# Kernel optimization log

Measured on AMD Instinct MI355X. Metric: run time of the kernel, lower is better.

## Reference

```python
import jax, jax.numpy as jnp
from jax import lax
import numpy as np

EPS = 1e-5
RADIUS = 0.2
NPOINT = 1024
NSAMPLE = 32
B, N = 8, 8192


def furthest_point_sample(xyz, npoint):
    # xyz: (B,N,3) -> idx (B,npoint), start at index 0 (pytorch3d default)
    Bn, Nn, _ = xyz.shape
    def step(carry, _):
        dists, last = carry  # (B,N), (B,)
        lastpt = jnp.take_along_axis(xyz, last[:, None, None], axis=1)  # (B,1,3)
        d = jnp.sum((xyz - lastpt) ** 2, axis=-1)  # (B,N)
        dists = jnp.minimum(dists, d)
        nxt = jnp.argmax(dists, axis=-1).astype(jnp.int32)
        return (dists, nxt), last
    init = (jnp.full((Bn, Nn), jnp.inf, xyz.dtype), jnp.zeros((Bn,), jnp.int32))
    _, idxs = lax.scan(step, init, None, length=npoint)  # (npoint,B)
    return idxs.T  # (B,npoint)


def ball_query(radius, nsample, xyz, new_xyz):
    # first `nsample` points (by original index order) within radius; pad -> 0 (clamp of -1)
    Nn = xyz.shape[1]
    d2 = jnp.sum((new_xyz[:, :, None, :] - xyz[:, None, :, :]) ** 2, axis=-1)  # (B,S,N)
    valid = d2 < radius * radius
    score = jnp.where(valid, jnp.arange(Nn, dtype=jnp.int32), jnp.int32(Nn))  # smaller = earlier valid
    neg_vals, _ = lax.top_k(-score, nsample)  # picks nsample smallest scores
    idx = -neg_vals  # (B,S,nsample)
    idx = jnp.where(idx == Nn, 0, idx)  # pytorch3d pads with -1, then clamp(min=0) -> 0
    return idx


def bn_relu(x, g, be, m, v):
    # eval-mode BatchNorm over channel (last) dim + ReLU
    return jax.nn.relu((x - m) * (g / jnp.sqrt(v + EPS)) + be)


def setup_inputs() -> dict:
    key = jax.random.key(0)
    ks = jax.random.split(key, 4)
    xyz = jax.random.uniform(ks[0], (B, N, 3), dtype=jnp.float32)
    w1 = jax.random.normal(ks[1], (64, 3), dtype=jnp.float32) * 0.1
    w2 = jax.random.normal(ks[2], (64, 64), dtype=jnp.float32) * 0.1
    w3 = jax.random.normal(ks[3], (128, 64), dtype=jnp.float32) * 0.1
    z64, o64 = jnp.zeros((64,), jnp.float32), jnp.ones((64,), jnp.float32)
    z128, o128 = jnp.zeros((128,), jnp.float32), jnp.ones((128,), jnp.float32)
    return {
        "xyz": xyz,
        "w1": w1, "b1": z64, "g1": o64, "be1": z64, "m1": z64, "v1": o64,
        "w2": w2, "b2": z64, "g2": o64, "be2": z64, "m2": z64, "v2": o64,
        "w3": w3, "b3": z128, "g3": o128, "be3": z128, "m3": z128, "v3": o128,
    }


def reference(xyz, w1, b1, g1, be1, m1, v1, w2, b2, g2, be2, m2, v2, w3, b3, g3, be3, m3, v3):
    fps_idx = furthest_point_sample(xyz, NPOINT)  # (B,npoint)
    new_xyz = jnp.take_along_axis(xyz, fps_idx[:, :, None], axis=1)  # (B,npoint,3)
    idx = ball_query(RADIUS, NSAMPLE, xyz, new_xyz)  # (B,npoint,nsample)
    grouped_xyz = jax.vmap(lambda pts, i: pts[i])(xyz, idx)  # (B,npoint,nsample,3)
    # 1x1 conv MLP (channels-last) + eval BN + ReLU
    h = bn_relu(jnp.einsum('bsnc,oc->bsno', grouped_xyz, w1) + b1, g1, be1, m1, v1)
    h = bn_relu(jnp.einsum('bsnc,oc->bsno', h, w2) + b2, g2, be2, m2, v2)
    h = bn_relu(jnp.einsum('bsnc,oc->bsno', h, w3) + b3, g3, be3, m3, v3)
    new_features = jnp.max(h, axis=2)  # (B,npoint,128) max over nsample
    new_features = jnp.transpose(new_features, (0, 2, 1))  # (B,128,npoint) to match torch layout
    return new_xyz, new_features
```

## Files before the change

### kernel.cpp

```cpp
#include <hip/hip_runtime.h>

#define B 8
#define N 8192
#define S 1024
#define NS 32
constexpr float BN_EPS = 1e-5f;

typedef float v2f __attribute__((ext_vector_type(2)));

__device__ __forceinline__ float wave_max_to_lane63(float x) {
  int v = __float_as_int(x);
#define DPP_MAX(ctrl)                                                     \
  v = __float_as_int(fmaxf(__int_as_float(v),                             \
      __int_as_float(__builtin_amdgcn_update_dpp(v, v, (ctrl), 0xf, 0xf, \
                                                 false))))
  DPP_MAX(0x111);
  DPP_MAX(0x112);
  DPP_MAX(0x114);
  DPP_MAX(0x118);
  DPP_MAX(0x142);
  DPP_MAX(0x143);
#undef DPP_MAX
  return __int_as_float(v);
}

#define FPS_T 512

__global__ void __attribute__((amdgpu_flat_work_group_size(FPS_T, FPS_T),
                               amdgpu_waves_per_eu(2, 2)))
k_fps(const float* __restrict__ xyz, float* __restrict__ new_xyz) {
#pragma clang fp contract(off)
  extern __shared__ float s_xyz[];
  const int b = blockIdx.x;
  const int t = threadIdx.x;
  const int lane = t & 63;
  const int w = t >> 6;
  const float* base = xyz + (size_t)b * N * 3;
  v2f X[8], Y[8], Z[8], D[8];
  const int p0 = t * 16;
  {
    const float4* src = (const float4*)(base + (size_t)p0 * 3);
    float4* dst = (float4*)(s_xyz + (size_t)p0 * 3);
    float buf[48];
#pragma unroll
    for (int i = 0; i < 12; ++i) {
      float4 v = src[i];
      dst[i] = v;
      buf[4 * i + 0] = v.x; buf[4 * i + 1] = v.y;
      buf[4 * i + 2] = v.z; buf[4 * i + 3] = v.w;
    }
#pragma unroll
    for (int i = 0; i < 8; ++i) {
      X[i] = (v2f){buf[6 * i + 0], buf[6 * i + 3]};
      Y[i] = (v2f){buf[6 * i + 1], buf[6 * i + 4]};
      Z[i] = (v2f){buf[6 * i + 2], buf[6 * i + 5]};
      D[i] = (v2f){3.4e38f, 3.4e38f};
    }
  }
  __shared__ unsigned long long s_red[2][8];
  float lx = base[0], ly = base[1], lz = base[2];
  if (t == 0) {
    float* o = new_xyz + (size_t)b * S * 3;
    o[0] = lx; o[1] = ly; o[2] = lz;
  }
  for (int r = 1; r < S; ++r) {
    v2f lx2 = lx, ly2 = ly, lz2 = lz;
#pragma unroll
    for (int i = 0; i < 8; ++i) {
      v2f dx = X[i] - lx2, dy = Y[i] - ly2, dz = Z[i] - lz2;
      v2f d = (dx * dx + dy * dy) + dz * dz;
      D[i].x = fminf(D[i].x, d.x);
      D[i].y = fminf(D[i].y, d.y);
    }
    float m = fmaxf(D[0].x, D[0].y);
#pragma unroll
    for (int i = 1; i < 8; ++i) m = fmaxf(m, fmaxf(D[i].x, D[i].y));
    int li = 0;
#pragma unroll
    for (int i = 7; i >= 0; --i) {
      if (D[i].y == m) li = 2 * i + 1;
      if (D[i].x == m) li = 2 * i;
    }
    float wm = wave_max_to_lane63(m);
    float wavemax = __int_as_float(
        __builtin_amdgcn_readlane(__float_as_int(wm), 63));
    unsigned long long bal = __ballot(m == wavemax);
    int firstlane = (int)__builtin_ctzll(bal);
    int widx = __builtin_amdgcn_readlane(p0 + li, firstlane);
    unsigned long long key =
        ((unsigned long long)__float_as_uint(wavemax) << 32) |
        (unsigned)(8191 - widx);
    if (lane == 0) s_red[r & 1][w] = key;
    __syncthreads();
    unsigned long long k0 = s_red[r & 1][0];
#pragma unroll
    for (int j = 1; j < 8; ++j) {
      unsigned long long kj = s_red[r & 1][j];
      if (kj > k0) k0 = kj;
    }
    const int bi = 8191 - (int)(unsigned)(k0 & 0xffffffffull);
    lx = s_xyz[bi * 3 + 0];
    ly = s_xyz[bi * 3 + 1];
    lz = s_xyz[bi * 3 + 2];
    if (t == 0) {
      float* o = new_xyz + ((size_t)b * S + r) * 3;
      o[0] = lx; o[1] = ly; o[2] = lz;
    }
  }
}

__global__ __launch_bounds__(256) void k_ball(const float* __restrict__ xyz,
                                              const float* __restrict__ new_xyz,
                                              int* __restrict__ ball_idx) {
#pragma clang fp contract(off)
  constexpr float R2 = (float)(0.2 * 0.2);
  const int t = threadIdx.x;
  const int wv = (blockIdx.x << 2) + (t >> 6);
  const int lane = t & 63;
  const int b = wv >> 10;
  const float* base = xyz + (size_t)b * N * 3;
  const float* c = new_xyz + (size_t)wv * 3;
  float cx = c[0], cy = c[1], cz = c[2];
  int* out = ball_idx + (size_t)wv * NS;
  int cnt = 0;
  for (int c0 = 0; c0 < N && cnt < NS; c0 += 64) {
    int p = c0 + lane;
    float x = base[p * 3], y = base[p * 3 + 1], z = base[p * 3 + 2];
    float dx = x - cx, dy = y - cy, dz = z - cz;
    float d = (dx * dx + dy * dy) + dz * dz;
    bool v = d < R2;
    unsigned long long mk = __ballot(v);
    int rank = cnt + __popcll(mk & ((1ull << lane) - 1ull));
    if (v && rank < NS) out[rank] = p;
    cnt += (int)__popcll(mk);
  }
  if (cnt < NS)
    for (int j = cnt + lane; j < NS; j += 64) out[j] = 0;
}

__global__ void __attribute__((amdgpu_flat_work_group_size(256, 256),
                               amdgpu_waves_per_eu(2, 2)))
k_mlp(const float* __restrict__ xyz, const int* __restrict__ ball_idx,
      const float* __restrict__ w1, const float* __restrict__ b1,
      const float* __restrict__ g1, const float* __restrict__ be1,
      const float* __restrict__ m1, const float* __restrict__ v1,
      const float* __restrict__ w2, const float* __restrict__ b2,
      const float* __restrict__ g2, const float* __restrict__ be2,
      const float* __restrict__ m2, const float* __restrict__ v2,
      const float* __restrict__ w3, const float* __restrict__ b3,
      const float* __restrict__ g3, const float* __restrict__ be3,
      const float* __restrict__ m3, const float* __restrict__ v3,
      float* __restrict__ out_feat) {
  const int t = threadIdx.x;
  const int w = t >> 6, lane = t & 63;
  const int wv = (blockIdx.x << 2) + w;
  const int b = wv >> 10, s = wv & (S - 1);
  __shared__ float sh[4][NS * 64];
  __shared__ float sc[4][NS * 4];
  float* h = sh[w];
  float* cs = sc[w];
  const int* gi = ball_idx + (size_t)wv * NS;
  const float* base = xyz + (size_t)b * N * 3;
  if (lane < NS) {
    int p = gi[lane];
    cs[lane * 4 + 0] = base[p * 3 + 0];
    cs[lane * 4 + 1] = base[p * 3 + 1];
    cs[lane * 4 + 2] = base[p * 3 + 2];
  }
  __syncthreads();
  {
    float sv = g1[lane] / sqrtf(v1[lane] + BN_EPS);
    float bb = (b1[lane] - m1[lane]) * sv + be1[lane];
    float wx = w1[lane * 3 + 0] * sv, wy = w1[lane * 3 + 1] * sv,
          wz = w1[lane * 3 + 2] * sv;
    for (int n = 0; n < NS; ++n) {
      float a = fmaf(wx, cs[n * 4 + 0],
                     fmaf(wy, cs[n * 4 + 1], fmaf(wz, cs[n * 4 + 2], bb)));
      h[n * 64 + lane] = fmaxf(a, 0.f);
    }
  }
  __syncthreads();
  {
    float sv = g2[lane] / sqrtf(v2[lane] + BN_EPS);
    float bb = (b2[lane] - m2[lane]) * sv + be2[lane];
    float W[64];
#pragma unroll
    for (int k = 0; k < 64; k += 4) {
      float4 q = *(const float4*)(w2 + lane * 64 + k);
      W[k + 0] = q.x * sv; W[k + 1] = q.y * sv;
      W[k + 2] = q.z * sv; W[k + 3] = q.w * sv;
    }
    for (int n = 0; n < NS; ++n) {
      float acc = bb;
#pragma unroll
      for (int k = 0; k < 64; k += 4) {
        float4 q = *(const float4*)(h + n * 64 + k);
        acc = fmaf(W[k + 0], q.x, acc);
        acc = fmaf(W[k + 1], q.y, acc);
        acc = fmaf(W[k + 2], q.z, acc);
        acc = fmaf(W[k + 3], q.w, acc);
      }
      h[n * 64 + lane] = fmaxf(acc, 0.f);
    }
  }
  __syncthreads();
  float mxa = 0.f, mxb = 0.f;
  {
    float sva = g3[lane] / sqrtf(v3[lane] + BN_EPS);
    float bba = (b3[lane] - m3[lane]) * sva + be3[lane];
    float svb = g3[lane + 64] / sqrtf(v3[lane + 64] + BN_EPS);
    float bbb = (b3[lane + 64] - m3[lane + 64]) * svb + be3[lane + 64];
    float Wa[64], Wb[64];
#pragma unroll
    for (int k = 0; k < 64; k += 4) {
      float4 qa = *(const float4*)(w3 + lane * 64 + k);
      Wa[k + 0] = qa.x * sva; Wa[k + 1] = qa.y * sva;
      Wa[k + 2] = qa.z * sva; Wa[k + 3] = qa.w * sva;
      float4 qb = *(const float4*)(w3 + (lane + 64) * 64 + k);
      Wb[k + 0] = qb.x * svb; Wb[k + 1] = qb.y * svb;
      Wb[k + 2] = qb.z * svb; Wb[k + 3] = qb.w * svb;
    }
    for (int n = 0; n < NS; ++n) {
      float acca = bba, accb = bbb;
#pragma unroll
      for (int k = 0; k < 64; k += 4) {
        float4 q = *(const float4*)(h + n * 64 + k);
        acca = fmaf(Wa[k + 0], q.x, acca);
        acca = fmaf(Wa[k + 1], q.y, acca);
        acca = fmaf(Wa[k + 2], q.z, acca);
        acca = fmaf(Wa[k + 3], q.w, acca);
        accb = fmaf(Wb[k + 0], q.x, accb);
        accb = fmaf(Wb[k + 1], q.y, accb);
        accb = fmaf(Wb[k + 2], q.z, accb);
        accb = fmaf(Wb[k + 3], q.w, accb);
      }
      mxa = fmaxf(mxa, acca);
      mxb = fmaxf(mxb, accb);
    }
  }
  out_feat[((size_t)b * 128 + lane) * S + s] = mxa;
  out_feat[((size_t)b * 128 + 64 + lane) * S + s] = mxb;
}

extern "C" void kernel_launch(void* const* d_in, const int* in_sizes, int n_in,
                              void* d_out, int out_size, void* d_ws,
                              size_t ws_size, hipStream_t stream) {
  const float* xyz = (const float*)d_in[0];
  const float* w1 = (const float*)d_in[1];
  const float* b1 = (const float*)d_in[2];
  const float* g1 = (const float*)d_in[3];
  const float* be1 = (const float*)d_in[4];
  const float* m1 = (const float*)d_in[5];
  const float* v1 = (const float*)d_in[6];
  const float* w2 = (const float*)d_in[7];
  const float* b2 = (const float*)d_in[8];
  const float* g2 = (const float*)d_in[9];
  const float* be2 = (const float*)d_in[10];
  const float* m2 = (const float*)d_in[11];
  const float* v2 = (const float*)d_in[12];
  const float* w3 = (const float*)d_in[13];
  const float* b3 = (const float*)d_in[14];
  const float* g3 = (const float*)d_in[15];
  const float* be3 = (const float*)d_in[16];
  const float* m3 = (const float*)d_in[17];
  const float* v3 = (const float*)d_in[18];

  float* out = (float*)d_out;
  float* new_xyz = out;
  float* out_feat = out + (size_t)B * S * 3;
  int* ball = (int*)d_ws;

  k_fps<<<B, FPS_T, N * 3 * sizeof(float), stream>>>(xyz, new_xyz);
  k_ball<<<(B * S) / 4, 256, 0, stream>>>(xyz, new_xyz, ball);
  k_mlp<<<(B * S) / 4, 256, 0, stream>>>(xyz, ball, w1, b1, g1, be1, m1, v1,
                                         w2, b2, g2, be2, m2, v2, w3, b3, g3,
                                         be3, m3, v3, out_feat);
}
```

Measured before the change: 1.113 ms.

## Shorten FPS iteration critical path with tree argmax and padded float4 LDS

```diff
diff --git a/kernel.cpp b/kernel.cpp
--- a/kernel.cpp
+++ b/kernel.cpp
@@ -30,7 +30,9 @@
                                amdgpu_waves_per_eu(2, 2)))
 k_fps(const float* __restrict__ xyz, float* __restrict__ new_xyz) {
 #pragma clang fp contract(off)
-  extern __shared__ float s_xyz[];
+  extern __shared__ float4 s_xyz4[];
+  __shared__ alignas(16) float s_ctr[S * 3];
+  __shared__ unsigned long long s_red[2][8];
   const int b = blockIdx.x;
   const int t = threadIdx.x;
   const int lane = t & 63;
@@ -40,14 +42,17 @@
   const int p0 = t * 16;
   {
     const float4* src = (const float4*)(base + (size_t)p0 * 3);
-    float4* dst = (float4*)(s_xyz + (size_t)p0 * 3);
     float buf[48];
 #pragma unroll
     for (int i = 0; i < 12; ++i) {
       float4 v = src[i];
-      dst[i] = v;
       buf[4 * i + 0] = v.x; buf[4 * i + 1] = v.y;
       buf[4 * i + 2] = v.z; buf[4 * i + 3] = v.w;
+    }
+#pragma unroll
+    for (int k = 0; k < 16; ++k) {
+      s_xyz4[p0 + k] =
+          make_float4(buf[3 * k], buf[3 * k + 1], buf[3 * k + 2], 0.f);
     }
 #pragma unroll
     for (int i = 0; i < 8; ++i) {
@@ -57,11 +62,9 @@
       D[i] = (v2f){3.4e38f, 3.4e38f};
     }
   }
-  __shared__ unsigned long long s_red[2][8];
   float lx = base[0], ly = base[1], lz = base[2];
   if (t == 0) {
-    float* o = new_xyz + (size_t)b * S * 3;
-    o[0] = lx; o[1] = ly; o[2] = lz;
+    s_ctr[0] = lx; s_ctr[1] = ly; s_ctr[2] = lz;
   }
   for (int r = 1; r < S; ++r) {
     v2f lx2 = lx, ly2 = ly, lz2 = lz;
@@ -69,18 +72,32 @@
     for (int i = 0; i < 8; ++i) {
       v2f dx = X[i] - lx2, dy = Y[i] - ly2, dz = Z[i] - lz2;
       v2f d = (dx * dx + dy * dy) + dz * dz;
-      D[i].x = fminf(D[i].x, d.x);
-      D[i].y = fminf(D[i].y, d.y);
-    }
-    float m = fmaxf(D[0].x, D[0].y);
-#pragma unroll
-    for (int i = 1; i < 8; ++i) m = fmaxf(m, fmaxf(D[i].x, D[i].y));
-    int li = 0;
-#pragma unroll
-    for (int i = 7; i >= 0; --i) {
-      if (D[i].y == m) li = 2 * i + 1;
-      if (D[i].x == m) li = 2 * i;
-    }
+      D[i] = __builtin_elementwise_min(D[i], d);
+    }
+    float n1[8], n2[4], n3[2];
+#pragma unroll
+    for (int i = 0; i < 8; ++i) n1[i] = fmaxf(D[i].x, D[i].y);
+#pragma unroll
+    for (int i = 0; i < 4; ++i) n2[i] = fmaxf(n1[2 * i], n1[2 * i + 1]);
+    n3[0] = fmaxf(n2[0], n2[1]);
+    n3[1] = fmaxf(n2[2], n2[3]);
+    float m = fmaxf(n3[0], n3[1]);
+    int c3 = (n3[0] < m) ? 1 : 0;
+    float n2s = c3 ? n2[2] : n2[0];
+    int c2 = (n2s < m) ? 1 : 0;
+    float n1a = c3 ? n1[4] : n1[0];
+    float n1b = c3 ? n1[6] : n1[2];
+    float n1s = c2 ? n1b : n1a;
+    int c1 = (n1s < m) ? 1 : 0;
+    float dx0 = c3 ? D[4].x : D[0].x;
+    float dx1 = c3 ? D[5].x : D[1].x;
+    float dx2 = c3 ? D[6].x : D[2].x;
+    float dx3 = c3 ? D[7].x : D[3].x;
+    float dxa = c2 ? dx2 : dx0;
+    float dxb = c2 ? dx3 : dx1;
+    float dxs = c1 ? dxb : dxa;
+    int c0 = (dxs < m) ? 1 : 0;
+    int li = 8 * c3 + 4 * c2 + 2 * c1 + c0;
     float wm = wave_max_to_lane63(m);
     float wavemax = __int_as_float(
         __builtin_amdgcn_readlane(__float_as_int(wm), 63));
@@ -92,20 +109,29 @@
         (unsigned)(8191 - widx);
     if (lane == 0) s_red[r & 1][w] = key;
     __syncthreads();
-    unsigned long long k0 = s_red[r & 1][0];
-#pragma unroll
-    for (int j = 1; j < 8; ++j) {
-      unsigned long long kj = s_red[r & 1][j];
-      if (kj > k0) k0 = kj;
-    }
-    const int bi = 8191 - (int)(unsigned)(k0 & 0xffffffffull);
-    lx = s_xyz[bi * 3 + 0];
-    ly = s_xyz[bi * 3 + 1];
-    lz = s_xyz[bi * 3 + 2];
+    {
+      const unsigned long long* sr = s_red[r & 1];
+      unsigned long long k0 = sr[0], k1 = sr[1], k2 = sr[2], k3 = sr[3];
+      unsigned long long k4 = sr[4], k5 = sr[5], k6 = sr[6], k7 = sr[7];
+      unsigned long long a = k0 > k1 ? k0 : k1;
+      unsigned long long c = k2 > k3 ? k2 : k3;
+      unsigned long long e = k4 > k5 ? k4 : k5;
+      unsigned long long g = k6 > k7 ? k6 : k7;
+      unsigned long long ac = a > c ? a : c;
+      unsigned long long eg = e > g ? e : g;
+      unsigned long long kmax = ac > eg ? ac : eg;
+      const int bi = 8191 - (int)(unsigned)(kmax & 0xffffffffull);
+      float4 cc = s_xyz4[bi];
+      lx = cc.x; ly = cc.y; lz = cc.z;
+    }
     if (t == 0) {
-      float* o = new_xyz + ((size_t)b * S + r) * 3;
-      o[0] = lx; o[1] = ly; o[2] = lz;
-    }
+      s_ctr[r * 3 + 0] = lx; s_ctr[r * 3 + 1] = ly; s_ctr[r * 3 + 2] = lz;
+    }
+  }
+  __syncthreads();
+  float* o = new_xyz + (size_t)b * S * 3;
+  for (int i = t; i < (S * 3) / 4; i += FPS_T) {
+    ((float4*)o)[i] = ((const float4*)s_ctr)[i];
   }
 }
 
@@ -270,7 +296,7 @@
   float* out_feat = out + (size_t)B * S * 3;
   int* ball = (int*)d_ws;
 
-  k_fps<<<B, FPS_T, N * 3 * sizeof(float), stream>>>(xyz, new_xyz);
+  k_fps<<<B, FPS_T, N * sizeof(float4), stream>>>(xyz, new_xyz);
   k_ball<<<(B * S) / 4, 256, 0, stream>>>(xyz, new_xyz, ball);
   k_mlp<<<(B * S) / 4, 256, 0, stream>>>(xyz, ball, w1, b1, g1, be1, m1, v1,
                                          w2, b2, g2, be2, m2, v2, w3, b3, g3,
```

Result: faster. 1.066 ms (-4.2%).
